# Kernel optimization log

Hardware: AMD Instinct MI355X
Metric: run time of the kernel (lower is better)

## Reference

```python
import jax, jax.numpy as jnp
import numpy as np

B, L, C, K = 32, 32768, 128, 64  # batch, length, channels(=filters), taps

def setup_inputs() -> dict:
    key = jax.random.key(0)
    k1, k2, k3 = jax.random.split(key, 3)
    x = jax.random.normal(k1, (B, L, C), dtype=jnp.float32)
    # Keras kernel shape: (kernel_size, 1, filters)
    kernel = jax.random.normal(k2, (K, 1, C), dtype=jnp.float32) * 0.05
    bias = jax.random.normal(k3, (C,), dtype=jnp.float32) * 0.05
    return {"x": x, "kernel": kernel, "bias": bias}

def reference(x, kernel, bias):
    # The original loops per filter: out[..., i] = conv1d(x[..., i:i+1], kernel[:, :, i:i+1]).
    # This is exactly a depthwise conv1d (feature_group_count = C), done here in one fused call.
    c = x.shape[-1]
    out = jax.lax.conv_general_dilated(
        x, kernel,
        window_strides=(1,),
        padding="SAME",  # TF 'same' with stride 1: total pad K-1, low=floor/high=ceil -> matches XLA SAME
        rhs_dilation=(1,),
        dimension_numbers=("NWC", "WIO", "NWC"),
        feature_group_count=c,
    )
    return jnp.tanh(out + bias)
```

## Files before the change

### kernel.cpp

```cpp
#include <hip/hip_runtime.h>
#include <cstdint>
#include <cstddef>


#define BQ 32
#define LQ 32768
#define CQ 128
#define KQ 64
#define NSTRIP 16
#define SLEN (LQ / NSTRIP)
#define CHUNK 32
#define NCH (SLEN / CHUNK)
#define RING 128
#define RPT 16

typedef const __attribute__((address_space(1))) unsigned int gas1_u32;
typedef __attribute__((address_space(3))) unsigned int las3_u32;

__global__ __launch_bounds__(256, 2) void dwconv_tanh_kernel(
    const float* __restrict__ x, const float* __restrict__ kern,
    const float* __restrict__ bias, float* __restrict__ out) {
  __shared__ __align__(16) float xs[RING * CQ];

  const int tid = threadIdx.x;
  const int c   = tid & 127;
  const int h   = tid >> 7;
  const int b   = blockIdx.x >> 4;
  const int s   = blockIdx.x & (NSTRIP - 1);
  const int t_s = s * SLEN;
  const bool firstStrip = (s == 0);
  const bool lastStrip  = (s == NSTRIP - 1);

  const float* xb = x + (size_t)b * (LQ * CQ);

  float w[KQ];
#pragma unroll
  for (int k = 0; k < KQ; ++k) w[k] = kern[k * CQ + c];
  const float bc = bias[c];

  auto stage = [&](int j) {
    const int T = t_s - 32 + 32 * j;
    const unsigned slot0 = (96u + 32u * (unsigned)j) & 127u;
#pragma unroll
    for (int u = 0; u < 4; ++u) {
      const int off  = u * 4096 + tid * 16;
      const int trow = off >> 9;
      const int cb   = off & 511;
      int t = T + trow;
      t = t < 0 ? 0 : (t >= LQ ? LQ - 1 : t);
      const float* gp = xb + (size_t)t * CQ + (cb >> 2);
      float* lp = &xs[(slot0 + (unsigned)trow) * CQ + (unsigned)(cb >> 2)];
      __builtin_amdgcn_global_load_lds((gas1_u32*)gp, (las3_u32*)lp, 16, 0, 0);
    }
  };

  stage(0); stage(1); stage(2);
  __syncthreads();
  if (firstStrip) {
#pragma unroll
    for (int u = 0; u < 16; ++u) xs[96 * CQ + u * 256 + tid] = 0.f;
    __syncthreads();
  }

  for (int i = 0; i < NCH; ++i) {
    if ((i < NCH - 1) && !(lastStrip && i == NCH - 2)) {
      stage(i + 3);
      asm volatile("s_waitcnt vmcnt(20)" ::: "memory");
    } else {
      asm volatile("s_waitcnt vmcnt(16)" ::: "memory");
    }

    if (lastStrip && i == NCH - 1) {
#pragma unroll
      for (int u = 0; u < 16; ++u) xs[u * 256 + tid] = 0.f;
      asm volatile("s_waitcnt lgkmcnt(0)" ::: "memory");
    }

    asm volatile("" ::: "memory");
    __builtin_amdgcn_s_barrier();
    asm volatile("" ::: "memory");

    const int t0 = t_s + CHUNK * i + RPT * h;
    float acc[RPT];
#pragma unroll
    for (int r = 0; r < RPT; ++r) acc[r] = 0.f;

    const unsigned base = (((unsigned)(t0 + 97) & 127u) << 9) + ((unsigned)c << 2);
    const char* xsb = (const char*)xs;
#pragma unroll
    for (int ii = 0; ii < RPT + KQ - 1; ++ii) {
      const unsigned a = (base + (unsigned)(ii * 512)) & 65535u;
      const float v = *(const float*)(xsb + a);
#pragma unroll
      for (int r = 0; r < RPT; ++r) {
        const int k = ii - r;
        if (k >= 0 && k < KQ) acc[r] = fmaf(w[k], v, acc[r]);
      }
    }

    float* op = out + ((size_t)b * LQ + (size_t)t0) * CQ + c;
#pragma unroll
    for (int r = 0; r < RPT; ++r) {
      const float z = acc[r] + bc;
      const float e = __expf(2.0f * z);
      op[(size_t)r * CQ] = 1.0f - 2.0f * __builtin_amdgcn_rcpf(e + 1.0f);
    }

    asm volatile("" ::: "memory");
    __builtin_amdgcn_s_barrier();
    asm volatile("" ::: "memory");
  }
}

extern "C" void kernel_launch(void* const* d_in, const int* in_sizes, int n_in,
                              void* d_out, int out_size, void* d_ws, size_t ws_size,
                              hipStream_t stream) {
  const float* x    = (const float*)d_in[0];
  const float* kern = (const float*)d_in[1];
  const float* bias = (const float*)d_in[2];
  float* out        = (float*)d_out;
  dwconv_tanh_kernel<<<dim3(BQ * NSTRIP), dim3(256), 0, stream>>>(x, kern, bias, out);
}
```

Baseline: 913.4 us.

## Split channels into two groups, mirror ring tail for immediate-offset LDS reads

Each block now handles 64 channels instead of 128, doubling the grid and halving per-block LDS so four blocks can fit per CU. The ring buffer gets a mirrored tail region so the convolution window can be read with compile-time immediate offsets without wraparound masking, and the chunk loop is unrolled by four to make slot offsets constant. Rows per thread drop from 16 to 8, which means more redundant LDS reads per output and extra mirror-copy work and barriers in exchange for higher occupancy and cheaper addressing.

After: 887.6 us. 1.03x faster.

```diff
diff --git a/kernel.cpp b/kernel.cpp
--- a/kernel.cpp
+++ b/kernel.cpp
@@ -6,109 +6,139 @@
 #define BQ 32
 #define LQ 32768
 #define CQ 128
+#define BC 64
 #define KQ 64
 #define NSTRIP 16
 #define SLEN (LQ / NSTRIP)
 #define CHUNK 32
 #define NCH (SLEN / CHUNK)
-#define RING 128
-#define RPT 16
+#define RINGB 32768
+#define MIRB 6144
+#define RPT 8
 
 typedef const __attribute__((address_space(1))) unsigned int gas1_u32;
 typedef __attribute__((address_space(3))) unsigned int las3_u32;
 
-__global__ __launch_bounds__(256, 2) void dwconv_tanh_kernel(
+__global__ __launch_bounds__(256, 4) void dwconv_tanh_kernel(
     const float* __restrict__ x, const float* __restrict__ kern,
     const float* __restrict__ bias, float* __restrict__ out) {
-  __shared__ __align__(16) float xs[RING * CQ];
+  __shared__ __align__(16) float xs[(RINGB + MIRB) / 4];
 
   const int tid = threadIdx.x;
-  const int c   = tid & 127;
-  const int h   = tid >> 7;
-  const int b   = blockIdx.x >> 4;
-  const int s   = blockIdx.x & (NSTRIP - 1);
+  const int c   = tid & (BC - 1);
+  const int h   = tid >> 6;
+  const int bid = blockIdx.x;
+  const int cg  = bid & 1;
+  const int s   = (bid >> 1) & (NSTRIP - 1);
+  const int b   = bid >> 5;
   const int t_s = s * SLEN;
   const bool firstStrip = (s == 0);
   const bool lastStrip  = (s == NSTRIP - 1);
 
-  const float* xb = x + (size_t)b * (LQ * CQ);
+  const float* xb = x + (size_t)b * (LQ * CQ) + cg * BC;
 
   float w[KQ];
 #pragma unroll
-  for (int k = 0; k < KQ; ++k) w[k] = kern[k * CQ + c];
-  const float bc = bias[c];
+  for (int k = 0; k < KQ; ++k) w[k] = kern[k * CQ + cg * BC + c];
+  const float bc = bias[cg * BC + c];
 
-  auto stage = [&](int j) {
-    const int T = t_s - 32 + 32 * j;
-    const unsigned slot0 = (96u + 32u * (unsigned)j) & 127u;
+  auto stage = [&](int j, int srowbyte) {
 #pragma unroll
-    for (int u = 0; u < 4; ++u) {
+    for (int u = 0; u < 2; ++u) {
       const int off  = u * 4096 + tid * 16;
-      const int trow = off >> 9;
-      const int cb   = off & 511;
-      int t = T + trow;
+      const int trow = off >> 8;
+      const int cb   = off & 255;
+      int t = t_s - 32 + 32 * j + trow;
       t = t < 0 ? 0 : (t >= LQ ? LQ - 1 : t);
       const float* gp = xb + (size_t)t * CQ + (cb >> 2);
-      float* lp = &xs[(slot0 + (unsigned)trow) * CQ + (unsigned)(cb >> 2)];
+      float* lp = (float*)((char*)xs + srowbyte + off);
       __builtin_amdgcn_global_load_lds((gas1_u32*)gp, (las3_u32*)lp, 16, 0, 0);
     }
   };
 
-  stage(0); stage(1); stage(2);
+  stage(0, 24576); stage(1, 0); stage(2, 8192);
   __syncthreads();
+  const int o0 = tid * 16;
   if (firstStrip) {
+    const float4 z4 = {0.f, 0.f, 0.f, 0.f};
+    *(float4*)((char*)xs + 24576 + o0) = z4;
+    *(float4*)((char*)xs + 28672 + o0) = z4;
+  }
+  {
+    float4 a0 = *(const float4*)((const char*)xs + o0);
+    *(float4*)((char*)xs + RINGB + o0) = a0;
+    if (tid < 128) {
+      float4 a1 = *(const float4*)((const char*)xs + 4096 + o0);
+      *(float4*)((char*)xs + RINGB + 4096 + o0) = a1;
+    }
+  }
+  __syncthreads();
+
+  for (int io = 0; io < NCH / 4; ++io) {
 #pragma unroll
-    for (int u = 0; u < 16; ++u) xs[96 * CQ + u * 256 + tid] = 0.f;
-    __syncthreads();
-  }
+    for (int jj = 0; jj < 4; ++jj) {
+      const int i = io * 4 + jj;
+      const int slotb = ((64 + 32 * jj) & 127) * 256;
+      const bool doStage = (i < NCH - 1) && !(lastStrip && i == NCH - 2);
+      if (doStage) {
+        stage(i + 3, slotb);
+        asm volatile("s_waitcnt vmcnt(10)" ::: "memory");
+      } else {
+        asm volatile("s_waitcnt vmcnt(8)" ::: "memory");
+      }
 
-  for (int i = 0; i < NCH; ++i) {
-    if ((i < NCH - 1) && !(lastStrip && i == NCH - 2)) {
-      stage(i + 3);
-      asm volatile("s_waitcnt vmcnt(20)" ::: "memory");
-    } else {
-      asm volatile("s_waitcnt vmcnt(16)" ::: "memory");
-    }
+      if (jj == 3) {
+        if (lastStrip && i == NCH - 1) {
+          const float4 z4 = {0.f, 0.f, 0.f, 0.f};
+          *(float4*)((char*)xs + o0) = z4;
+          *(float4*)((char*)xs + 4096 + o0) = z4;
+          *(float4*)((char*)xs + RINGB + o0) = z4;
+          if (tid < 128) *(float4*)((char*)xs + RINGB + 4096 + o0) = z4;
+        } else {
+          float4 a0 = *(const float4*)((const char*)xs + o0);
+          *(float4*)((char*)xs + RINGB + o0) = a0;
+          if (tid < 128) {
+            float4 a1 = *(const float4*)((const char*)xs + 4096 + o0);
+            *(float4*)((char*)xs + RINGB + 4096 + o0) = a1;
+          }
+        }
+        asm volatile("s_waitcnt lgkmcnt(0)" ::: "memory");
+      }
 
-    if (lastStrip && i == NCH - 1) {
+      asm volatile("" ::: "memory");
+      __builtin_amdgcn_s_barrier();
+      asm volatile("" ::: "memory");
+
+      const int t0 = t_s + CHUNK * i + RPT * h;
+      float acc[RPT];
 #pragma unroll
-      for (int u = 0; u < 16; ++u) xs[u * 256 + tid] = 0.f;
-      asm volatile("s_waitcnt lgkmcnt(0)" ::: "memory");
-    }
+      for (int r = 0; r < RPT; ++r) acc[r] = 0.f;
 
-    asm volatile("" ::: "memory");
-    __builtin_amdgcn_s_barrier();
-    asm volatile("" ::: "memory");
+      const char* xsb = (const char*)xs;
+      const unsigned vb = ((unsigned)h << 11) + ((unsigned)c << 2);
+#pragma unroll
+      for (int ii = 0; ii < RPT + KQ - 1; ++ii) {
+        const int imm = ((32 * jj + 97 + ii) & 127) * 256;
+        const float v = *(const float*)(xsb + vb + imm);
+#pragma unroll
+        for (int r = 0; r < RPT; ++r) {
+          const int k = ii - r;
+          if (k >= 0 && k < KQ) acc[r] = fmaf(w[k], v, acc[r]);
+        }
+      }
 
-    const int t0 = t_s + CHUNK * i + RPT * h;
-    float acc[RPT];
-#pragma unroll
-    for (int r = 0; r < RPT; ++r) acc[r] = 0.f;
-
-    const unsigned base = (((unsigned)(t0 + 97) & 127u) << 9) + ((unsigned)c << 2);
-    const char* xsb = (const char*)xs;
-#pragma unroll
-    for (int ii = 0; ii < RPT + KQ - 1; ++ii) {
-      const unsigned a = (base + (unsigned)(ii * 512)) & 65535u;
-      const float v = *(const float*)(xsb + a);
+      float* op = out + ((size_t)b * LQ + (size_t)t0) * CQ + cg * BC + c;
 #pragma unroll
       for (int r = 0; r < RPT; ++r) {
-        const int k = ii - r;
-        if (k >= 0 && k < KQ) acc[r] = fmaf(w[k], v, acc[r]);
+        const float z = acc[r] + bc;
+        const float e = __expf(2.0f * z);
+        op[(size_t)r * CQ] = 1.0f - 2.0f * __builtin_amdgcn_rcpf(e + 1.0f);
       }
+
+      asm volatile("" ::: "memory");
+      __builtin_amdgcn_s_barrier();
+      asm volatile("" ::: "memory");
     }
-
-    float* op = out + ((size_t)b * LQ + (size_t)t0) * CQ + c;
-#pragma unroll
-    for (int r = 0; r < RPT; ++r) {
-      const float z = acc[r] + bc;
-      const float e = __expf(2.0f * z);
-      op[(size_t)r * CQ] = 1.0f - 2.0f * __builtin_amdgcn_rcpf(e + 1.0f);
-    }
-
-    asm volatile("" ::: "memory");
-    __builtin_amdgcn_s_barrier();
-    asm volatile("" ::: "memory");
   }
 }
 
@@ -119,5 +149,5 @@
   const float* kern = (const float*)d_in[1];
   const float* bias = (const float*)d_in[2];
   float* out        = (float*)d_out;
-  dwconv_tanh_kernel<<<dim3(BQ * NSTRIP), dim3(256), 0, stream>>>(x, kern, bias, out);
+  dwconv_tanh_kernel<<<dim3(BQ * NSTRIP * 2), dim3(256), 0, stream>>>(x, kern, bias, out);
 }
```
